# Optimization experiments

Hardware: AMD Instinct MI355X
Metric: run time of the kernel (lower is better)

The kernel has to match this reference:

```python
import jax, jax.numpy as jnp
import numpy as np

B, D, U, C = 256, 1024, 1024, 64


def setup_inputs() -> dict:
    key = jax.random.key(0)
    k1, k2, k3 = jax.random.split(key, 3)
    content_idx = jax.random.randint(k1, (B,), 0, C, dtype=jnp.int32)
    x = jax.random.normal(k2, (B, D), dtype=jnp.float32)
    embeddings = jax.random.normal(k3, (C, D, U), dtype=jnp.float32) * 0.02
    return {"content_idx": content_idx, "x": x, "embeddings": embeddings}


def reference(content_idx, x, embeddings):
    # Gather a (D, U) weight matrix per example, then per-example matvec:
    # out[b, u] = sum_d x[b, d] * embeddings[content_idx[b], d, u]
    w = embeddings[content_idx]              # [B, D, U]
    out = jnp.einsum('bd,bdu->bu', x, w)     # [B, U]
    return out
```

## Files before the change

### kernel.cpp

```cpp
#include <hip/hip_runtime.h>


#define B_N 256
#define D_N 1024
#define U_N 1024
#define C_N 64
#define MC  12
#define NW  16
#define TPB 1024

__device__ __forceinline__ void fma4(float4& a, const float4& e, float s) {
    a.x = fmaf(e.x, s, a.x);
    a.y = fmaf(e.y, s, a.y);
    a.z = fmaf(e.z, s, a.z);
    a.w = fmaf(e.w, s, a.w);
}

__global__ __launch_bounds__(TPB, 4) void content_gather_gemv(
    const int* __restrict__ idx,
    const float* __restrict__ x,
    const float* __restrict__ emb,
    float* __restrict__ out)
{
    __shared__ __align__(16) float smem[MC * D_N];
    __shared__ int bs[B_N];
    __shared__ int cnt;

    const int c    = blockIdx.x;
    const int ut   = blockIdx.y;
    const int tid  = threadIdx.x;
    const int wave = tid >> 6;
    const int lane = tid & 63;

    if (tid == 0) cnt = 0;
    __syncthreads();
    if (tid < B_N && idx[tid] == c) {
        bs[atomicAdd(&cnt, 1)] = tid;
    }
    __syncthreads();
    const int M = cnt;
    if (M == 0) return;

    const int u0 = ut * 256 + lane * 4;
    const int d0 = wave * (D_N / NW);
    const float* ebase = emb + ((size_t)c * D_N + d0) * U_N + u0;

    for (int base = 0; base < M; base += MC) {
        const int mc = min(MC, M - base);

        #pragma unroll
        for (int j = 0; j < MC; ++j) {
            float v = 0.f;
            if (j < mc) v = x[(size_t)bs[base + j] * D_N + tid];
            smem[j * D_N + tid] = v;
        }
        __syncthreads();

        float4 acc[MC];
        #pragma unroll
        for (int j = 0; j < MC; ++j) acc[j] = make_float4(0.f, 0.f, 0.f, 0.f);

        const bool m4 = (mc > 4);
        const bool m8 = (mc > 8);

        const float* ep = ebase;
        for (int dg = 0; dg < (D_N / NW) / 4; ++dg) {
            float4 e0 = *(const float4*)(ep);
            float4 e1 = *(const float4*)(ep + U_N);
            float4 e2 = *(const float4*)(ep + 2 * U_N);
            float4 e3 = *(const float4*)(ep + 3 * U_N);
            ep += 4 * U_N;
            const int dx = d0 + dg * 4;

            #pragma unroll
            for (int j = 0; j < 4; ++j) {
                float4 xv = *(const float4*)&smem[j * D_N + dx];
                fma4(acc[j], e0, xv.x); fma4(acc[j], e1, xv.y);
                fma4(acc[j], e2, xv.z); fma4(acc[j], e3, xv.w);
            }
            if (m4) {
                #pragma unroll
                for (int j = 4; j < 8; ++j) {
                    float4 xv = *(const float4*)&smem[j * D_N + dx];
                    fma4(acc[j], e0, xv.x); fma4(acc[j], e1, xv.y);
                    fma4(acc[j], e2, xv.z); fma4(acc[j], e3, xv.w);
                }
            }
            if (m8) {
                #pragma unroll
                for (int j = 8; j < MC; ++j) {
                    float4 xv = *(const float4*)&smem[j * D_N + dx];
                    fma4(acc[j], e0, xv.x); fma4(acc[j], e1, xv.y);
                    fma4(acc[j], e2, xv.z); fma4(acc[j], e3, xv.w);
                }
            }
        }

        __syncthreads();

        float4* red = (float4*)smem;
        #pragma unroll
        for (int j = 0; j < MC; ++j) {
            if (j < mc) {
                red[tid] = acc[j];
                __syncthreads();
                if (tid < 64) {
                    float4 s = red[tid];
                    #pragma unroll
                    for (int w = 1; w < NW; ++w) {
                        float4 a = red[w * 64 + tid];
                        s.x += a.x; s.y += a.y; s.z += a.z; s.w += a.w;
                    }
                    *(float4*)(out + (size_t)bs[base + j] * U_N + ut * 256 + tid * 4) = s;
                }
                __syncthreads();
            }
        }
        __syncthreads();
    }
}

extern "C" void kernel_launch(void* const* d_in, const int* in_sizes, int n_in,
                              void* d_out, int out_size, void* d_ws, size_t ws_size,
                              hipStream_t stream) {
    const int*   idx = (const int*)d_in[0];
    const float* x   = (const float*)d_in[1];
    const float* emb = (const float*)d_in[2];
    float*       out = (float*)d_out;

    dim3 grid(C_N, U_N / 256);
    dim3 block(TPB);
    content_gather_gemv<<<grid, block, 0, stream>>>(idx, x, emb, out);
}
```

Measured before the change: 46.51 us.

## Halve block size and U tile, use float2 lanes, parallelize cross-wave reduction

Blocks shrink from 1024 to 512 threads and each covers 128 output columns with float2 per lane, so the grid doubles to 512 blocks for better CU occupancy and load balance. The per-example reduction now writes all accumulators to shared memory once, and different waves reduce different examples in parallel, replacing the serialized one-example-per-barrier loop. In exchange each lane issues narrower 8-byte global loads, and every block repeats the x staging and index scan.

```diff
diff --git a/kernel.cpp b/kernel.cpp
--- a/kernel.cpp
+++ b/kernel.cpp
@@ -6,14 +6,13 @@
 #define U_N 1024
 #define C_N 64
 #define MC  12
-#define NW  16
-#define TPB 1024
+#define NW  8
+#define TPB 512
+#define UT  128
 
-__device__ __forceinline__ void fma4(float4& a, const float4& e, float s) {
+__device__ __forceinline__ void fma2(float2& a, const float2& e, float s) {
     a.x = fmaf(e.x, s, a.x);
     a.y = fmaf(e.y, s, a.y);
-    a.z = fmaf(e.z, s, a.z);
-    a.w = fmaf(e.w, s, a.w);
 }
 
 __global__ __launch_bounds__(TPB, 4) void content_gather_gemv(
@@ -41,7 +40,7 @@
     const int M = cnt;
     if (M == 0) return;
 
-    const int u0 = ut * 256 + lane * 4;
+    const int u0 = ut * UT + lane * 2;
     const int d0 = wave * (D_N / NW);
     const float* ebase = emb + ((size_t)c * D_N + d0) * U_N + u0;
 
@@ -50,70 +49,72 @@
 
         #pragma unroll
         for (int j = 0; j < MC; ++j) {
-            float v = 0.f;
-            if (j < mc) v = x[(size_t)bs[base + j] * D_N + tid];
-            smem[j * D_N + tid] = v;
+            float2 v = make_float2(0.f, 0.f);
+            if (j < mc) v = *(const float2*)(x + (size_t)bs[base + j] * D_N + tid * 2);
+            *(float2*)&smem[j * D_N + tid * 2] = v;
         }
         __syncthreads();
 
-        float4 acc[MC];
+        float2 acc[MC];
         #pragma unroll
-        for (int j = 0; j < MC; ++j) acc[j] = make_float4(0.f, 0.f, 0.f, 0.f);
+        for (int j = 0; j < MC; ++j) acc[j] = make_float2(0.f, 0.f);
 
         const bool m4 = (mc > 4);
         const bool m8 = (mc > 8);
 
         const float* ep = ebase;
         for (int dg = 0; dg < (D_N / NW) / 4; ++dg) {
-            float4 e0 = *(const float4*)(ep);
-            float4 e1 = *(const float4*)(ep + U_N);
-            float4 e2 = *(const float4*)(ep + 2 * U_N);
-            float4 e3 = *(const float4*)(ep + 3 * U_N);
+            float2 e0 = *(const float2*)(ep);
+            float2 e1 = *(const float2*)(ep + U_N);
+            float2 e2 = *(const float2*)(ep + 2 * U_N);
+            float2 e3 = *(const float2*)(ep + 3 * U_N);
             ep += 4 * U_N;
             const int dx = d0 + dg * 4;
 
             #pragma unroll
             for (int j = 0; j < 4; ++j) {
                 float4 xv = *(const float4*)&smem[j * D_N + dx];
-                fma4(acc[j], e0, xv.x); fma4(acc[j], e1, xv.y);
-                fma4(acc[j], e2, xv.z); fma4(acc[j], e3, xv.w);
+                fma2(acc[j], e0, xv.x); fma2(acc[j], e1, xv.y);
+                fma2(acc[j], e2, xv.z); fma2(acc[j], e3, xv.w);
             }
             if (m4) {
                 #pragma unroll
                 for (int j = 4; j < 8; ++j) {
                     float4 xv = *(const float4*)&smem[j * D_N + dx];
-                    fma4(acc[j], e0, xv.x); fma4(acc[j], e1, xv.y);
-                    fma4(acc[j], e2, xv.z); fma4(acc[j], e3, xv.w);
+                    fma2(acc[j], e0, xv.x); fma2(acc[j], e1, xv.y);
+                    fma2(acc[j], e2, xv.z); fma2(acc[j], e3, xv.w);
                 }
             }
             if (m8) {
                 #pragma unroll
                 for (int j = 8; j < MC; ++j) {
                     float4 xv = *(const float4*)&smem[j * D_N + dx];
-                    fma4(acc[j], e0, xv.x); fma4(acc[j], e1, xv.y);
-                    fma4(acc[j], e2, xv.z); fma4(acc[j], e3, xv.w);
+                    fma2(acc[j], e0, xv.x); fma2(acc[j], e1, xv.y);
+                    fma2(acc[j], e2, xv.z); fma2(acc[j], e3, xv.w);
                 }
             }
         }
 
         __syncthreads();
 
-        float4* red = (float4*)smem;
+        float2* red = (float2*)smem;
         #pragma unroll
         for (int j = 0; j < MC; ++j) {
-            if (j < mc) {
-                red[tid] = acc[j];
-                __syncthreads();
-                if (tid < 64) {
-                    float4 s = red[tid];
-                    #pragma unroll
-                    for (int w = 1; w < NW; ++w) {
-                        float4 a = red[w * 64 + tid];
-                        s.x += a.x; s.y += a.y; s.z += a.z; s.w += a.w;
-                    }
-                    *(float4*)(out + (size_t)bs[base + j] * U_N + ut * 256 + tid * 4) = s;
+            if (j < mc) red[j * TPB + tid] = acc[j];
+        }
+        __syncthreads();
+
+        #pragma unroll
+        for (int rep = 0; rep < 2; ++rep) {
+            const int j = wave + rep * NW;
+            if (j < mc && (rep == 0 || wave < 4)) {
+                float2 s = red[j * TPB + lane];
+                #pragma unroll
+                for (int w = 1; w < NW; ++w) {
+                    float2 a = red[j * TPB + w * 64 + lane];
+                    s.x += a.x; s.y += a.y;
                 }
-                __syncthreads();
+                *(float2*)(out + (size_t)bs[base + j] * U_N + ut * UT + lane * 2) = s;
             }
         }
         __syncthreads();
@@ -128,7 +129,7 @@
     const float* emb = (const float*)d_in[2];
     float*       out = (float*)d_out;
 
-    dim3 grid(C_N, U_N / 256);
+    dim3 grid(C_N, U_N / UT);
     dim3 block(TPB);
     content_gather_gemv<<<grid, block, 0, stream>>>(idx, x, emb, out);
 }
```

Result: no change. 47.30 us (+1.7%).

## Split the D reduction across blocks and accumulate outputs with float atomics

Applied to the files above, without the earlier changes.

The work is regridded so that each block handles one content index and one slice of D, with 256 threads each covering four U columns across the full U range. This replaces the earlier U-tiled blocks and their in-block 16-wave shared-memory reduction. Partial sums are added into the output with unsafe float atomics after a memset of the output. The intended gain is less shared memory, fewer barriers and smaller blocks, at the cost of extra atomic traffic, an extra memset launch and run-to-run nondeterminism in summation order.

```diff
diff --git a/kernel.cpp b/kernel.cpp
--- a/kernel.cpp
+++ b/kernel.cpp
@@ -6,8 +6,9 @@
 #define U_N 1024
 #define C_N 64
 #define MC  12
-#define NW  16
-#define TPB 1024
+#define TPB 256
+#define DC_N 8
+#define DCHUNK (D_N / DC_N)
 
 __device__ __forceinline__ void fma4(float4& a, const float4& e, float s) {
     a.x = fmaf(e.x, s, a.x);
@@ -16,43 +17,50 @@
     a.w = fmaf(e.w, s, a.w);
 }
 
-__global__ __launch_bounds__(TPB, 4) void content_gather_gemv(
+__device__ __forceinline__ void atom_add_f(float* p, float v) {
+#if defined(__AMDGCN__)
+    unsafeAtomicAdd(p, v);
+#else
+    atomicAdd(p, v);
+#endif
+}
+
+__global__ __launch_bounds__(TPB) void content_dsplit(
     const int* __restrict__ idx,
     const float* __restrict__ x,
     const float* __restrict__ emb,
     float* __restrict__ out)
 {
-    __shared__ __align__(16) float smem[MC * D_N];
+    __shared__ __align__(16) float xs[MC][DCHUNK];
     __shared__ int bs[B_N];
     __shared__ int cnt;
 
-    const int c    = blockIdx.x;
-    const int ut   = blockIdx.y;
-    const int tid  = threadIdx.x;
-    const int wave = tid >> 6;
-    const int lane = tid & 63;
+    const int c   = blockIdx.x;
+    const int dc  = blockIdx.y;
+    const int tid = threadIdx.x;
 
     if (tid == 0) cnt = 0;
     __syncthreads();
-    if (tid < B_N && idx[tid] == c) {
+    if (idx[tid] == c) {
         bs[atomicAdd(&cnt, 1)] = tid;
     }
     __syncthreads();
     const int M = cnt;
     if (M == 0) return;
 
-    const int u0 = ut * 256 + lane * 4;
-    const int d0 = wave * (D_N / NW);
-    const float* ebase = emb + ((size_t)c * D_N + d0) * U_N + u0;
+    const int d0 = dc * DCHUNK;
+    const int u0 = tid * 4;
 
     for (int base = 0; base < M; base += MC) {
         const int mc = min(MC, M - base);
 
         #pragma unroll
         for (int j = 0; j < MC; ++j) {
-            float v = 0.f;
-            if (j < mc) v = x[(size_t)bs[base + j] * D_N + tid];
-            smem[j * D_N + tid] = v;
+            if (tid < DCHUNK) {
+                float v = 0.f;
+                if (j < mc) v = x[(size_t)bs[base + j] * D_N + d0 + tid];
+                xs[j][tid] = v;
+            }
         }
         __syncthreads();
 
@@ -63,25 +71,24 @@
         const bool m4 = (mc > 4);
         const bool m8 = (mc > 8);
 
-        const float* ep = ebase;
-        for (int dg = 0; dg < (D_N / NW) / 4; ++dg) {
+        const float* ep = emb + ((size_t)c * D_N + d0) * U_N + u0;
+        for (int dg = 0; dg < DCHUNK / 4; ++dg) {
             float4 e0 = *(const float4*)(ep);
             float4 e1 = *(const float4*)(ep + U_N);
             float4 e2 = *(const float4*)(ep + 2 * U_N);
             float4 e3 = *(const float4*)(ep + 3 * U_N);
             ep += 4 * U_N;
-            const int dx = d0 + dg * 4;
 
             #pragma unroll
             for (int j = 0; j < 4; ++j) {
-                float4 xv = *(const float4*)&smem[j * D_N + dx];
+                float4 xv = *(const float4*)&xs[j][dg * 4];
                 fma4(acc[j], e0, xv.x); fma4(acc[j], e1, xv.y);
                 fma4(acc[j], e2, xv.z); fma4(acc[j], e3, xv.w);
             }
             if (m4) {
                 #pragma unroll
                 for (int j = 4; j < 8; ++j) {
-                    float4 xv = *(const float4*)&smem[j * D_N + dx];
+                    float4 xv = *(const float4*)&xs[j][dg * 4];
                     fma4(acc[j], e0, xv.x); fma4(acc[j], e1, xv.y);
                     fma4(acc[j], e2, xv.z); fma4(acc[j], e3, xv.w);
                 }
@@ -89,31 +96,21 @@
             if (m8) {
                 #pragma unroll
                 for (int j = 8; j < MC; ++j) {
-                    float4 xv = *(const float4*)&smem[j * D_N + dx];
+                    float4 xv = *(const float4*)&xs[j][dg * 4];
                     fma4(acc[j], e0, xv.x); fma4(acc[j], e1, xv.y);
                     fma4(acc[j], e2, xv.z); fma4(acc[j], e3, xv.w);
                 }
             }
         }
 
-        __syncthreads();
-
-        float4* red = (float4*)smem;
         #pragma unroll
         for (int j = 0; j < MC; ++j) {
             if (j < mc) {
-                red[tid] = acc[j];
-                __syncthreads();
-                if (tid < 64) {
-                    float4 s = red[tid];
-                    #pragma unroll
-                    for (int w = 1; w < NW; ++w) {
-                        float4 a = red[w * 64 + tid];
-                        s.x += a.x; s.y += a.y; s.z += a.z; s.w += a.w;
-                    }
-                    *(float4*)(out + (size_t)bs[base + j] * U_N + ut * 256 + tid * 4) = s;
-                }
-                __syncthreads();
+                float* op = out + (size_t)bs[base + j] * U_N + u0;
+                atom_add_f(op + 0, acc[j].x);
+                atom_add_f(op + 1, acc[j].y);
+                atom_add_f(op + 2, acc[j].z);
+                atom_add_f(op + 3, acc[j].w);
             }
         }
         __syncthreads();
@@ -128,7 +125,9 @@
     const float* emb = (const float*)d_in[2];
     float*       out = (float*)d_out;
 
-    dim3 grid(C_N, U_N / 256);
+    hipMemsetAsync(out, 0, (size_t)out_size * sizeof(float), stream);
+
+    dim3 grid(C_N, DC_N);
     dim3 block(TPB);
-    content_gather_gemv<<<grid, block, 0, stream>>>(idx, x, emb, out);
+    content_dsplit<<<grid, block, 0, stream>>>(idx, x, emb, out);
 }
```

New measurement: 74.05 us. 59.2% more time.

## Split D across blocks with workspace partials and a separate reduction kernel

Applied to the files above, without the earlier changes.

Each block now covers all U columns for one quarter of the D rows. It writes partial sums to a workspace buffer, and a second small kernel adds the four partials into the output. Each block reads the selected x rows only once instead of once per U tile, and its cross-wave reduction shrinks from 16 waves to 4. Embedding loads now use nontemporal hints. The cost is an extra kernel launch and a 4 MB partial write and read. The old kernel stays as a fallback when the workspace is too small.

```diff
diff --git a/kernel.cpp b/kernel.cpp
--- a/kernel.cpp
+++ b/kernel.cpp
@@ -6,8 +6,11 @@
 #define U_N 1024
 #define C_N 64
 #define MC  12
-#define NW  16
-#define TPB 1024
+#define DC  4
+#define DROWS (D_N / DC)
+#define TPB1 1024
+
+typedef float f32x4 __attribute__((ext_vector_type(4)));
 
 __device__ __forceinline__ void fma4(float4& a, const float4& e, float s) {
     a.x = fmaf(e.x, s, a.x);
@@ -15,39 +18,151 @@
     a.z = fmaf(e.z, s, a.z);
     a.w = fmaf(e.w, s, a.w);
 }
-
-__global__ __launch_bounds__(TPB, 4) void content_gather_gemv(
+__device__ __forceinline__ float4 ntload4(const float* p) {
+    f32x4 v = __builtin_nontemporal_load((const f32x4*)p);
+    return make_float4(v.x, v.y, v.z, v.w);
+}
+
+__global__ __launch_bounds__(TPB1, 4) void content_partial(
     const int* __restrict__ idx,
     const float* __restrict__ x,
     const float* __restrict__ emb,
-    float* __restrict__ out)
+    float* __restrict__ part)
+{
+    __shared__ __align__(16) float xs[MC][DROWS];
+    __shared__ __align__(16) float4 red[4 * 256];
+    __shared__ int bs[B_N];
+    __shared__ int cnt;
+
+    const int c   = blockIdx.x;
+    const int dc  = blockIdx.y;
+    const int tid = threadIdx.x;
+    const int uq  = tid & 255;
+    const int ds  = tid >> 8;
+
+    if (tid == 0) cnt = 0;
+    __syncthreads();
+    if (tid < B_N && idx[tid] == c) {
+        bs[atomicAdd(&cnt, 1)] = tid;
+    }
+    __syncthreads();
+    const int M = cnt;
+    if (M == 0) return;
+
+    const int u0 = uq * 4;
+    const int drow0 = dc * DROWS + ds * (DROWS / 4);
+    const float* ebase = emb + ((size_t)c * D_N + drow0) * U_N + u0;
+
+    for (int base = 0; base < M; base += MC) {
+        const int mc = min(MC, M - base);
+
+        #pragma unroll
+        for (int jj = 0; jj < MC / 4; ++jj) {
+            const int j = jj * 4 + ds;
+            float v = 0.f;
+            if (j < mc) v = x[(size_t)bs[base + j] * D_N + dc * DROWS + uq];
+            xs[j][uq] = v;
+        }
+        __syncthreads();
+
+        float4 acc[MC];
+        #pragma unroll
+        for (int j = 0; j < MC; ++j) acc[j] = make_float4(0.f, 0.f, 0.f, 0.f);
+
+        const bool m4 = (mc > 4);
+        const bool m8 = (mc > 8);
+
+        const float* ep = ebase;
+        for (int dg = 0; dg < (DROWS / 4) / 4; ++dg) {
+            float4 e0 = ntload4(ep);
+            float4 e1 = ntload4(ep + U_N);
+            float4 e2 = ntload4(ep + 2 * U_N);
+            float4 e3 = ntload4(ep + 3 * U_N);
+            ep += 4 * U_N;
+            const int dl = ds * (DROWS / 4) + dg * 4;
+
+            #pragma unroll
+            for (int j = 0; j < 4; ++j) {
+                float4 xv = *(const float4*)&xs[j][dl];
+                fma4(acc[j], e0, xv.x); fma4(acc[j], e1, xv.y);
+                fma4(acc[j], e2, xv.z); fma4(acc[j], e3, xv.w);
+            }
+            if (m4) {
+                #pragma unroll
+                for (int j = 4; j < 8; ++j) {
+                    float4 xv = *(const float4*)&xs[j][dl];
+                    fma4(acc[j], e0, xv.x); fma4(acc[j], e1, xv.y);
+                    fma4(acc[j], e2, xv.z); fma4(acc[j], e3, xv.w);
+                }
+            }
+            if (m8) {
+                #pragma unroll
+                for (int j = 8; j < MC; ++j) {
+                    float4 xv = *(const float4*)&xs[j][dl];
+                    fma4(acc[j], e0, xv.x); fma4(acc[j], e1, xv.y);
+                    fma4(acc[j], e2, xv.z); fma4(acc[j], e3, xv.w);
+                }
+            }
+        }
+
+        #pragma unroll
+        for (int j = 0; j < MC; ++j) {
+            if (j < mc) {
+                red[ds * 256 + uq] = acc[j];
+                __syncthreads();
+                if (ds == 0) {
+                    float4 a0 = red[uq];
+                    float4 a1 = red[256 + uq];
+                    float4 a2 = red[512 + uq];
+                    float4 a3 = red[768 + uq];
+                    float4 s;
+                    s.x = (a0.x + a1.x) + (a2.x + a3.x);
+                    s.y = (a0.y + a1.y) + (a2.y + a3.y);
+                    s.z = (a0.z + a1.z) + (a2.z + a3.z);
+                    s.w = (a0.w + a1.w) + (a2.w + a3.w);
+                    *(float4*)(part + ((size_t)dc * B_N + bs[base + j]) * U_N + u0) = s;
+                }
+                __syncthreads();
+            }
+        }
+        __syncthreads();
+    }
+}
+
+__global__ __launch_bounds__(256) void content_reduce(
+    const float* __restrict__ part, float* __restrict__ out)
+{
+    const int i = blockIdx.x * 256 + threadIdx.x;
+    const f32x4* p = (const f32x4*)part;
+    f32x4 a = __builtin_nontemporal_load(p + i);
+    f32x4 b = __builtin_nontemporal_load(p + 65536 + i);
+    f32x4 c = __builtin_nontemporal_load(p + 131072 + i);
+    f32x4 d = __builtin_nontemporal_load(p + 196608 + i);
+    f32x4 s = (a + b) + (c + d);
+    ((f32x4*)out)[i] = s;
+}
+
+#define NW_FB 16
+__global__ __launch_bounds__(1024, 4) void content_fb(
+    const int* __restrict__ idx, const float* __restrict__ x,
+    const float* __restrict__ emb, float* __restrict__ out)
 {
     __shared__ __align__(16) float smem[MC * D_N];
     __shared__ int bs[B_N];
     __shared__ int cnt;
-
-    const int c    = blockIdx.x;
-    const int ut   = blockIdx.y;
-    const int tid  = threadIdx.x;
-    const int wave = tid >> 6;
-    const int lane = tid & 63;
-
+    const int c = blockIdx.x, ut = blockIdx.y, tid = threadIdx.x;
+    const int wave = tid >> 6, lane = tid & 63;
     if (tid == 0) cnt = 0;
     __syncthreads();
-    if (tid < B_N && idx[tid] == c) {
-        bs[atomicAdd(&cnt, 1)] = tid;
-    }
+    if (tid < B_N && idx[tid] == c) bs[atomicAdd(&cnt, 1)] = tid;
     __syncthreads();
     const int M = cnt;
     if (M == 0) return;
-
     const int u0 = ut * 256 + lane * 4;
-    const int d0 = wave * (D_N / NW);
+    const int d0 = wave * (D_N / NW_FB);
     const float* ebase = emb + ((size_t)c * D_N + d0) * U_N + u0;
-
     for (int base = 0; base < M; base += MC) {
         const int mc = min(MC, M - base);
-
         #pragma unroll
         for (int j = 0; j < MC; ++j) {
             float v = 0.f;
@@ -55,23 +170,18 @@
             smem[j * D_N + tid] = v;
         }
         __syncthreads();
-
         float4 acc[MC];
         #pragma unroll
         for (int j = 0; j < MC; ++j) acc[j] = make_float4(0.f, 0.f, 0.f, 0.f);
-
-        const bool m4 = (mc > 4);
-        const bool m8 = (mc > 8);
-
+        const bool m4 = (mc > 4), m8 = (mc > 8);
         const float* ep = ebase;
-        for (int dg = 0; dg < (D_N / NW) / 4; ++dg) {
+        for (int dg = 0; dg < (D_N / NW_FB) / 4; ++dg) {
             float4 e0 = *(const float4*)(ep);
             float4 e1 = *(const float4*)(ep + U_N);
             float4 e2 = *(const float4*)(ep + 2 * U_N);
             float4 e3 = *(const float4*)(ep + 3 * U_N);
             ep += 4 * U_N;
             const int dx = d0 + dg * 4;
-
             #pragma unroll
             for (int j = 0; j < 4; ++j) {
                 float4 xv = *(const float4*)&smem[j * D_N + dx];
@@ -95,9 +205,7 @@
                 }
             }
         }
-
-        __syncthreads();
-
+        __syncthreads();
         float4* red = (float4*)smem;
         #pragma unroll
         for (int j = 0; j < MC; ++j) {
@@ -107,7 +215,7 @@
                 if (tid < 64) {
                     float4 s = red[tid];
                     #pragma unroll
-                    for (int w = 1; w < NW; ++w) {
+                    for (int w = 1; w < NW_FB; ++w) {
                         float4 a = red[w * 64 + tid];
                         s.x += a.x; s.y += a.y; s.z += a.z; s.w += a.w;
                     }
@@ -128,7 +236,14 @@
     const float* emb = (const float*)d_in[2];
     float*       out = (float*)d_out;
 
-    dim3 grid(C_N, U_N / 256);
-    dim3 block(TPB);
-    content_gather_gemv<<<grid, block, 0, stream>>>(idx, x, emb, out);
-}
+    const size_t need = (size_t)DC * B_N * U_N * sizeof(float);
+    if (ws_size >= need) {
+        float* part = (float*)d_ws;
+        dim3 g1(C_N, DC);
+        content_partial<<<g1, TPB1, 0, stream>>>(idx, x, emb, part);
+        content_reduce<<<256, 256, 0, stream>>>(part, out);
+    } else {
+        dim3 g(C_N, U_N / 256);
+        content_fb<<<g, 1024, 0, stream>>>(idx, x, emb, out);
+    }
+}
```

Measured after the change: 48.03 us. 1.03x slower.
